# Kernel tuning notes

Hardware: AMD Instinct MI355X
Metric: run time of the kernel (lower is better)

## Reference

```python
import math
import jax, jax.numpy as jnp
import numpy as np

HIDDEN = 2048
NUM_HEADS = 32
HEAD_DIM = HIDDEN // NUM_HEADS
NUM_BLOCKS = 4
INTER = 2 * HIDDEN
EPS = 1e-5
ROPE_THETA = 10000.0


def setup_inputs() -> dict:
    key = jax.random.key(0)
    ks = jax.random.split(key, 6)
    B, S = 2, 2048
    sc = 0.02
    return {
        "x": jax.random.normal(ks[0], (B, S, HIDDEN), jnp.float32),
        "attn_norm_w": jnp.ones((HIDDEN,), jnp.float32),
        "ffn_norm_w": jnp.ones((HIDDEN,), jnp.float32),
        "w_qkv": jax.random.normal(ks[1], (3 * HIDDEN, HIDDEN), jnp.float32) * sc,
        "w_o": jax.random.normal(ks[2], (HIDDEN, HIDDEN), jnp.float32) * sc,
        "w_up": jax.random.normal(ks[3], (2 * INTER, HIDDEN), jnp.float32) * sc,
        "w_down": jax.random.normal(ks[4], (HIDDEN, INTER), jnp.float32) * sc,
    }


def _rmsnorm(x, w):
    var = jnp.mean(x * x, axis=-1, keepdims=True)
    return x * jax.lax.rsqrt(var + EPS) * w


def _rope_cache(seq_len, dim, theta, scale):
    inv_freq = 1.0 / (theta ** (jnp.arange(0, dim, 2, dtype=jnp.float32) / dim))
    t = jnp.arange(seq_len, dtype=jnp.float32) / scale
    freqs = jnp.outer(t, inv_freq)                     # [S, D/2]
    emb = jnp.concatenate([freqs, freqs], axis=-1)     # [S, D]
    return jnp.cos(emb), jnp.sin(emb)


def _apply_rope(x, cos, sin):
    # x: [B, H, S, D]
    d2 = x.shape[-1] // 2
    x1, x2 = x[..., :d2], x[..., d2:]
    rot = jnp.concatenate([-x2, x1], axis=-1)
    return x * cos[None, None] + rot * sin[None, None]


def reference(x, attn_norm_w, ffn_norm_w, w_qkv, w_o, w_up, w_down):
    B, S, _ = x.shape
    residual = x
    h = _rmsnorm(x, attn_norm_w)

    qkv = jnp.einsum('bsh,oh->bso', h, w_qkv)
    qkv = qkv.reshape(B, S, 3, NUM_HEADS, HEAD_DIM)
    q, k, v = qkv[:, :, 0], qkv[:, :, 1], qkv[:, :, 2]
    q = q.transpose(0, 2, 1, 3)  # [B,H,S,D]
    k = k.transpose(0, 2, 1, 3)
    v = v.transpose(0, 2, 1, 3)

    cos, sin = _rope_cache(S, HEAD_DIM, ROPE_THETA, 1.0)
    q = _apply_rope(q, cos, sin)
    k = _apply_rope(k, cos, sin)

    scale = 1.0 / math.sqrt(HEAD_DIM)
    attn = jnp.einsum('bhqd,bhkd->bhqk', q, k) * scale

    num_blocks = max(1, min(NUM_BLOCKS, S))
    blk = math.ceil(S / num_blocks)
    pos = jnp.arange(S)
    block_ids = pos // blk
    block_mask = block_ids[:, None] != block_ids[None, :]
    causal_mask = pos[:, None] < pos[None, :]
    invalid = causal_mask | block_mask                 # [S,S]
    mask_floor = jnp.finfo(attn.dtype).min
    attn = jnp.where(invalid[None, None], mask_floor, attn)

    attn = jax.nn.softmax(attn, axis=-1)
    context = jnp.einsum('bhqk,bhkd->bhqd', attn, v)
    context = context.transpose(0, 2, 1, 3).reshape(B, S, HIDDEN)

    x = residual + jnp.einsum('bsh,oh->bso', context, w_o)

    residual = x
    h = _rmsnorm(x, ffn_norm_w)
    up = jnp.einsum('bsh,oh->bso', h, w_up)
    gate, value = up[..., :INTER], up[..., INTER:]
    down = jnp.einsum('bsi,oi->bso', jax.nn.silu(gate) * value, w_down)
    return residual + down
```

## Files before the change

### kernel.cpp

```cpp
#include <hip/hip_runtime.h>
#include <cstdint>
#include <cstddef>

typedef __bf16 bf16x8 __attribute__((ext_vector_type(8)));
typedef __bf16 bf16x4 __attribute__((ext_vector_type(4)));
typedef float  f32x4  __attribute__((ext_vector_type(4)));

#define TOKENS  4096
#define SEQLEN  2048
#define HID     2048
#define QKV_W   6144
#define UP_W    8192
#define INTER_  4096

__device__ __forceinline__ void async16(const void* g, void* l) {
  __builtin_amdgcn_global_load_lds(
      (__attribute__((address_space(1))) void*)(g),
      (__attribute__((address_space(3))) void*)(l), 16, 0, 0);
}

__global__ __launch_bounds__(256) void cvt_kernel(const float* __restrict__ src,
                                                  __bf16* __restrict__ dst, int n4) {
  int i = blockIdx.x * 256 + threadIdx.x;
  if (i >= n4) return;
  float4 f = ((const float4*)src)[i];
  bf16x4 o;
  o[0] = (__bf16)f.x; o[1] = (__bf16)f.y; o[2] = (__bf16)f.z; o[3] = (__bf16)f.w;
  ((bf16x4*)dst)[i] = o;
}

__global__ __launch_bounds__(256) void rmsnorm_kernel(const float* __restrict__ x,
                                                      const float* __restrict__ wgt,
                                                      __bf16* __restrict__ out) {
  const int tok = blockIdx.x;
  const int t = threadIdx.x;
  const float4* xr = (const float4*)(x + (long)tok * HID);
  float4 a = xr[t], b = xr[t + 256];
  float ss = a.x*a.x + a.y*a.y + a.z*a.z + a.w*a.w
           + b.x*b.x + b.y*b.y + b.z*b.z + b.w*b.w;
  #pragma unroll
  for (int off = 32; off; off >>= 1) ss += __shfl_xor(ss, off);
  __shared__ float red[4];
  if ((t & 63) == 0) red[t >> 6] = ss;
  __syncthreads();
  float tot = red[0] + red[1] + red[2] + red[3];
  float r = rsqrtf(tot * (1.0f / HID) + 1e-5f);
  const float4* wr = (const float4*)wgt;
  float4 wa = wr[t], wb = wr[t + 256];
  bf16x4 o0, o1;
  o0[0] = (__bf16)(a.x * r * wa.x); o0[1] = (__bf16)(a.y * r * wa.y);
  o0[2] = (__bf16)(a.z * r * wa.z); o0[3] = (__bf16)(a.w * r * wa.w);
  o1[0] = (__bf16)(b.x * r * wb.x); o1[1] = (__bf16)(b.y * r * wb.y);
  o1[2] = (__bf16)(b.z * r * wb.z); o1[3] = (__bf16)(b.w * r * wb.w);
  bf16x4* orow = (bf16x4*)(out + (long)tok * HID);
  orow[t] = o0; orow[t + 256] = o1;
}

template<bool OUT_BF16, bool ADD_RES, bool ROPE, bool SILU>
__global__ __launch_bounds__(256) void gemm_bt(const __bf16* __restrict__ A, int lda,
                                               const __bf16* __restrict__ B, int ldb,
                                               void* Cv, int ldc,
                                               const float* __restrict__ Res, int K) {
  __shared__ __align__(16) __bf16 As[128 * 64];
  __shared__ __align__(16) __bf16 Bs[128 * 64];
  const int t = threadIdx.x;
  const int lane = t & 63;
  const int w = t >> 6;
  const int wm = (w >> 1) * 64, wn = (w & 1) * 64;
  const int m0 = blockIdx.y * 128;
  const int n0 = SILU ? blockIdx.x * 64 : blockIdx.x * 128;
  const int sr = t >> 3;
  const int sc = (((t & 7) ^ (sr & 7)) * 8);
  const __bf16* Ag = A + (long)(m0 + sr) * lda + sc;
  const __bf16* Bg = B + (long)(n0 + sr) * ldb + sc;
  char* lA = (char*)As + t * 16;
  char* lB = (char*)Bs + t * 16;
  const int lr = lane & 15;
  const int lq = lane >> 4;
  f32x4 acc[4][4] = {};
  for (int k0 = 0; k0 < K; k0 += 64) {
    __syncthreads();
    #pragma unroll
    for (int c = 0; c < 4; c++)
      async16(Ag + (long)(c * 32) * lda + k0, lA + c * 4096);
    #pragma unroll
    for (int c = 0; c < 4; c++) {
      const long rowoff = SILU ? (long)((c & 1) * INTER_ + (c >> 1) * 32) * ldb
                               : (long)(c * 32) * ldb;
      async16(Bg + rowoff + k0, lB + c * 4096);
    }
    __syncthreads();
    #pragma unroll
    for (int ks = 0; ks < 2; ks++) {
      const int pos = (((ks * 4 + lq) ^ (lr & 7)) * 8);
      bf16x8 af[4], bfr[4];
      #pragma unroll
      for (int i = 0; i < 4; i++)
        af[i]  = *(const bf16x8*)(As + (wm + i * 16 + lr) * 64 + pos);
      #pragma unroll
      for (int j = 0; j < 4; j++)
        bfr[j] = *(const bf16x8*)(Bs + (wn + j * 16 + lr) * 64 + pos);
      #pragma unroll
      for (int i = 0; i < 4; i++)
        #pragma unroll
        for (int j = 0; j < 4; j++)
          acc[i][j] = __builtin_amdgcn_mfma_f32_16x16x32_bf16(af[i], bfr[j], acc[i][j], 0, 0, 0);
    }
  }
  const int lq4 = lq * 4;
  if (ROPE && n0 < 4096) {
    const float invf0 = exp2f((float)(lr)      * -0.41524101186092029f);
    const float invf1 = exp2f((float)(16 + lr) * -0.41524101186092029f);
    #pragma unroll
    for (int i = 0; i < 4; i++) {
      #pragma unroll
      for (int r = 0; r < 4; r++) {
        const long row = m0 + wm + i * 16 + lq4 + r;
        const float s = (float)(int)(row & (SEQLEN - 1));
        __bf16* crow = (__bf16*)Cv + row * (long)ldc + n0 + wn + lr;
        #pragma unroll
        for (int j = 0; j < 2; j++) {
          float x1 = acc[i][j][r], x2 = acc[i][j + 2][r];
          float ang = s * (j ? invf1 : invf0);
          float sn, cs;
          __sincosf(ang, &sn, &cs);
          crow[j * 16]       = (__bf16)(x1 * cs - x2 * sn);
          crow[(j + 2) * 16] = (__bf16)(x2 * cs + x1 * sn);
        }
      }
    }
  } else if (SILU) {
    #pragma unroll
    for (int i = 0; i < 4; i++) {
      #pragma unroll
      for (int r = 0; r < 4; r++) {
        const long row = m0 + wm + i * 16 + lq4 + r;
        #pragma unroll
        for (int j = 0; j < 2; j++) {
          const long col = n0 + (wn >> 1) + j * 16 + lr;
          float g = acc[i][j][r];
          float v = acc[i][j + 2][r];
          float sg = g / (1.0f + __expf(-g));
          ((__bf16*)Cv)[row * (long)ldc + col] = (__bf16)(sg * v);
        }
      }
    }
  } else {
    #pragma unroll
    for (int i = 0; i < 4; i++) {
      #pragma unroll
      for (int r = 0; r < 4; r++) {
        const long row = m0 + wm + i * 16 + lq4 + r;
        #pragma unroll
        for (int j = 0; j < 4; j++) {
          const long col = n0 + wn + j * 16 + lr;
          float v = acc[i][j][r];
          if (ADD_RES) v += Res[row * (long)ldc + col];
          if (OUT_BF16) ((__bf16*)Cv)[row * (long)ldc + col] = (__bf16)v;
          else          ((float*)Cv)[row * (long)ldc + col] = v;
        }
      }
    }
  }
}

#define VTS 520
__global__ __launch_bounds__(256) void attn_kernel(const __bf16* __restrict__ qkv,
                                                   __bf16* __restrict__ ctx) {
  const int qt = blockIdx.x;
  const int h  = blockIdx.y;
  const int b  = blockIdx.z;
  const int w    = threadIdx.x >> 6;
  const int lane = threadIdx.x & 63;
  const int lr = lane & 15;
  const int lq = lane >> 4;
  const int q0   = qt * 64;
  const int blk0 = (q0 >> 9) << 9;
  const int nkv  = q0 + 64 - blk0;
  const long tok0 = (long)b * SEQLEN;

  const int qrow = q0 + w * 16 + lr;
  const long qoff = (tok0 + qrow) * QKV_W + h * 64 + lq * 8;
  bf16x8 qf0 = *(const bf16x8*)(qkv + qoff);
  bf16x8 qf1 = *(const bf16x8*)(qkv + qoff + 32);

  __shared__ __align__(16) __bf16 VT[64][VTS];
  __shared__ __align__(16) __bf16 Pb[4][16][48];

  {
    const int vc = (threadIdx.x & 7) * 8;
    for (int kv = threadIdx.x >> 3; kv < nkv; kv += 32) {
      bf16x8 v8 = *(const bf16x8*)(qkv + (tok0 + blk0 + kv) * QKV_W + 2 * HID + h * 64 + vc);
      #pragma unroll
      for (int i = 0; i < 8; i++) VT[vc + i][kv] = v8[i];
    }
  }
  __syncthreads();

  float m[4], l[4];
  f32x4 oacc[4] = {};
  #pragma unroll
  for (int r = 0; r < 4; r++) { m[r] = -1e30f; l[r] = 0.0f; }

  const int myrow = q0 + w * 16 + lq * 4;

  for (int kv0 = 0; kv0 < nkv; kv0 += 32) {
    f32x4 s[2];
    #pragma unroll
    for (int nt = 0; nt < 2; nt++) {
      const long koff = (tok0 + blk0 + kv0 + nt * 16 + lr) * QKV_W + HID + h * 64 + lq * 8;
      bf16x8 kf0 = *(const bf16x8*)(qkv + koff);
      bf16x8 kf1 = *(const bf16x8*)(qkv + koff + 32);
      f32x4 sa = {0.0f, 0.0f, 0.0f, 0.0f};
      sa = __builtin_amdgcn_mfma_f32_16x16x32_bf16(qf0, kf0, sa, 0, 0, 0);
      sa = __builtin_amdgcn_mfma_f32_16x16x32_bf16(qf1, kf1, sa, 0, 0, 0);
      const int kpos = blk0 + kv0 + nt * 16 + lr;
      #pragma unroll
      for (int r = 0; r < 4; r++) {
        float v = sa[r] * 0.125f;
        s[nt][r] = (kpos <= myrow + r) ? v : -1e30f;
      }
    }
    float p0[4], p1[4], alpha[4];
    #pragma unroll
    for (int r = 0; r < 4; r++) {
      float mx = fmaxf(s[0][r], s[1][r]);
      mx = fmaxf(mx, __shfl_xor(mx, 1));
      mx = fmaxf(mx, __shfl_xor(mx, 2));
      mx = fmaxf(mx, __shfl_xor(mx, 4));
      mx = fmaxf(mx, __shfl_xor(mx, 8));
      float mn = fmaxf(m[r], mx);
      alpha[r] = __expf(m[r] - mn);
      m[r] = mn;
      p0[r] = __expf(s[0][r] - mn);
      p1[r] = __expf(s[1][r] - mn);
      float rs = p0[r] + p1[r];
      rs += __shfl_xor(rs, 1);
      rs += __shfl_xor(rs, 2);
      rs += __shfl_xor(rs, 4);
      rs += __shfl_xor(rs, 8);
      l[r] = l[r] * alpha[r] + rs;
    }
    #pragma unroll
    for (int dt = 0; dt < 4; dt++)
      #pragma unroll
      for (int r = 0; r < 4; r++) oacc[dt][r] *= alpha[r];

    #pragma unroll
    for (int r = 0; r < 4; r++) {
      Pb[w][lq * 4 + r][lr]      = (__bf16)p0[r];
      Pb[w][lq * 4 + r][16 + lr] = (__bf16)p1[r];
    }
    asm volatile("s_waitcnt lgkmcnt(0)" ::: "memory");
    bf16x8 pf = *(const bf16x8*)(&Pb[w][lr][lq * 8]);
    #pragma unroll
    for (int dt = 0; dt < 4; dt++) {
      bf16x8 vf = *(const bf16x8*)(&VT[dt * 16 + lr][kv0 + lq * 8]);
      oacc[dt] = __builtin_amdgcn_mfma_f32_16x16x32_bf16(pf, vf, oacc[dt], 0, 0, 0);
    }
  }
  #pragma unroll
  for (int r = 0; r < 4; r++) {
    float inv = 1.0f / l[r];
    long obase = (tok0 + myrow + r) * HID + h * 64;
    #pragma unroll
    for (int dt = 0; dt < 4; dt++)
      ctx[obase + dt * 16 + lr] = (__bf16)(oacc[dt][r] * inv);
  }
}

extern "C" void kernel_launch(void* const* d_in, const int* in_sizes, int n_in,
                              void* d_out, int out_size, void* d_ws, size_t ws_size,
                              hipStream_t stream) {
  const float* x      = (const float*)d_in[0];
  const float* anw    = (const float*)d_in[1];
  const float* fnw    = (const float*)d_in[2];
  const float* w_qkv  = (const float*)d_in[3];
  const float* w_o    = (const float*)d_in[4];
  const float* w_up   = (const float*)d_in[5];
  const float* w_down = (const float*)d_in[6];
  float* out = (float*)d_out;

  char* wsb = (char*)d_ws;
  __bf16* ABUF = (__bf16*)wsb;
  __bf16* QKV  = (__bf16*)(wsb + (size_t)16777216);
  __bf16* WBUF = (__bf16*)(wsb + (size_t)83886080);
  __bf16* ACT  = QKV;

  rmsnorm_kernel<<<TOKENS, 256, 0, stream>>>(x, anw, ABUF);
  cvt_kernel<<<(QKV_W * HID / 4 + 255) / 256, 256, 0, stream>>>(w_qkv, WBUF, QKV_W * HID / 4);
  gemm_bt<true, false, true, false><<<dim3(QKV_W / 128, TOKENS / 128), 256, 0, stream>>>(
      ABUF, HID, WBUF, HID, (void*)QKV, QKV_W, nullptr, HID);
  attn_kernel<<<dim3(SEQLEN / 64, 32, 2), 256, 0, stream>>>(QKV, ABUF);
  cvt_kernel<<<(HID * HID / 4 + 255) / 256, 256, 0, stream>>>(w_o, WBUF, HID * HID / 4);
  gemm_bt<false, true, false, false><<<dim3(HID / 128, TOKENS / 128), 256, 0, stream>>>(
      ABUF, HID, WBUF, HID, (void*)out, HID, x, HID);

  rmsnorm_kernel<<<TOKENS, 256, 0, stream>>>(out, fnw, ABUF);
  cvt_kernel<<<(UP_W * HID / 4 + 255) / 256, 256, 0, stream>>>(w_up, WBUF, UP_W * HID / 4);
  gemm_bt<true, false, false, true><<<dim3(INTER_ / 64, TOKENS / 128), 256, 0, stream>>>(
      ABUF, HID, WBUF, HID, (void*)ACT, INTER_, nullptr, HID);
  cvt_kernel<<<(HID * INTER_ / 4 + 255) / 256, 256, 0, stream>>>(w_down, WBUF, HID * INTER_ / 4);
  gemm_bt<false, true, false, false><<<dim3(HID / 128, TOKENS / 128), 256, 0, stream>>>(
      ACT, INTER_, WBUF, INTER_, (void*)out, HID, out, INTER_);
}
```

Measured before the change: 617.9 us.

## Triple-buffer GEMM loads with 128x256 tiles, 512 threads and XCD-aware block remap

Rewrites the bf16 GEMM main loop so global-to-LDS async loads are issued two K-steps ahead into a three-stage ring buffer, waiting with vmcnt counts instead of a pair of full barriers per step. The block tile grows to 128x256 with 8 waves, and block indices are remapped in groups of 8, presumably to keep neighbouring tiles on the same XCD for L2 reuse. MFMA sections are wrapped in setprio. The aim is to hide load latency and raise operand reuse, at the cost of much more LDS (about 144KB) and register pressure, which limits occupancy.

```diff
diff --git a/kernel.cpp b/kernel.cpp
--- a/kernel.cpp
+++ b/kernel.cpp
@@ -57,56 +57,101 @@
 }
 
 template<bool OUT_BF16, bool ADD_RES, bool ROPE, bool SILU>
-__global__ __launch_bounds__(256) void gemm_bt(const __bf16* __restrict__ A, int lda,
-                                               const __bf16* __restrict__ B, int ldb,
-                                               void* Cv, int ldc,
-                                               const float* __restrict__ Res, int K) {
-  __shared__ __align__(16) __bf16 As[128 * 64];
-  __shared__ __align__(16) __bf16 Bs[128 * 64];
-  const int t = threadIdx.x;
-  const int lane = t & 63;
-  const int w = t >> 6;
-  const int wm = (w >> 1) * 64, wn = (w & 1) * 64;
-  const int m0 = blockIdx.y * 128;
-  const int n0 = SILU ? blockIdx.x * 64 : blockIdx.x * 128;
-  const int sr = t >> 3;
-  const int sc = (((t & 7) ^ (sr & 7)) * 8);
-  const __bf16* Ag = A + (long)(m0 + sr) * lda + sc;
-  const __bf16* Bg = B + (long)(n0 + sr) * ldb + sc;
-  char* lA = (char*)As + t * 16;
-  char* lB = (char*)Bs + t * 16;
-  const int lr = lane & 15;
-  const int lq = lane >> 4;
+__global__ __launch_bounds__(512, 2) void gemm_bt(const __bf16* __restrict__ A, int lda,
+                                                  const __bf16* __restrict__ B, int ldb,
+                                                  void* Cv, int ldc,
+                                                  const float* __restrict__ Res, int K) {
+  __shared__ __align__(16) __bf16 As[3 * 8192];
+  __shared__ __align__(16) __bf16 Bs[3 * 16384];
+  const int tid  = threadIdx.x;
+  const int lane = tid & 63;
+  const int w    = tid >> 6;
+  const int wm   = (w >> 2) * 64;
+  const int wn   = (w & 3) * 64;
+  const int lr   = lane & 15;
+  const int lq   = lane >> 4;
+
+  const int h   = blockIdx.y * gridDim.x + blockIdx.x;
+  const int per = (gridDim.x * gridDim.y) >> 3;
+  const int W   = (h & 7) * per + (h >> 3);
+  const int bx  = W / gridDim.y;
+  const int by  = W - bx * gridDim.y;
+  const int m0  = by * 128;
+  const int n0  = SILU ? bx * 128 : bx * 256;
+
+  const int srow = tid >> 2;
+  const int swz  = ((tid & 3) ^ ((tid >> 3) & 3)) * 8;
+  const __bf16* Ag = A + (long)(m0 + srow) * lda + swz;
+  long brow0, brow1;
+  if (SILU) {
+    const int R0 = srow, R1 = 128 + srow;
+    brow0 = (long)(((R0 >> 5) & 1) * INTER_ + n0 + (R0 >> 6) * 32 + (R0 & 31));
+    brow1 = (long)(((R1 >> 5) & 1) * INTER_ + n0 + (R1 >> 6) * 32 + (R1 & 31));
+  } else {
+    brow0 = n0 + srow;
+    brow1 = n0 + 128 + srow;
+  }
+  const __bf16* Bg0 = B + brow0 * ldb + swz;
+  const __bf16* Bg1 = B + brow1 * ldb + swz;
+  char* lA = (char*)As + tid * 16;
+  char* lB = (char*)Bs + tid * 16;
+
+#define STAGE(tt, bb) do {                                            \
+    const long ko_ = (long)(tt) * 64;                                 \
+    async16(Ag  + ko_,      lA + (bb) * 16384);                       \
+    async16(Ag  + ko_ + 32, lA + (bb) * 16384 + 8192);                \
+    async16(Bg0 + ko_,      lB + (bb) * 32768);                       \
+    async16(Bg1 + ko_,      lB + (bb) * 32768 + 8192);                \
+    async16(Bg0 + ko_ + 32, lB + (bb) * 32768 + 16384);               \
+    async16(Bg1 + ko_ + 32, lB + (bb) * 32768 + 16384 + 8192);        \
+  } while (0)
+
+  const int chx  = (lq ^ ((lr >> 1) & 3)) * 16;
+  const int aoff = (wm + lr) * 64 + chx;
+  const int boff = (wn + lr) * 64 + chx;
   f32x4 acc[4][4] = {};
-  for (int k0 = 0; k0 < K; k0 += 64) {
-    __syncthreads();
-    #pragma unroll
-    for (int c = 0; c < 4; c++)
-      async16(Ag + (long)(c * 32) * lda + k0, lA + c * 4096);
-    #pragma unroll
-    for (int c = 0; c < 4; c++) {
-      const long rowoff = SILU ? (long)((c & 1) * INTER_ + (c >> 1) * 32) * ldb
-                               : (long)(c * 32) * ldb;
-      async16(Bg + rowoff + k0, lB + c * 4096);
-    }
-    __syncthreads();
-    #pragma unroll
-    for (int ks = 0; ks < 2; ks++) {
-      const int pos = (((ks * 4 + lq) ^ (lr & 7)) * 8);
+  const int NT = K >> 6;
+
+  STAGE(0, 0);
+  STAGE(1, 1);
+  asm volatile("s_waitcnt vmcnt(6)" ::: "memory");
+  __builtin_amdgcn_sched_barrier(0);
+  __builtin_amdgcn_s_barrier();
+  asm volatile("" ::: "memory");
+
+  int bcur = 0;
+  for (int t = 0; t < NT; ++t) {
+    int bp = bcur + 2; if (bp >= 3) bp -= 3;
+    const bool pre = (t + 2 < NT);
+    if (pre) STAGE(t + 2, bp);
+    const char* Ab = (const char*)As + bcur * 16384;
+    const char* Bb = (const char*)Bs + bcur * 32768;
+    #pragma unroll
+    for (int ks = 0; ks < 2; ++ks) {
       bf16x8 af[4], bfr[4];
       #pragma unroll
       for (int i = 0; i < 4; i++)
-        af[i]  = *(const bf16x8*)(As + (wm + i * 16 + lr) * 64 + pos);
+        af[i]  = *(const bf16x8*)(Ab + ks * 8192  + aoff + i * 1024);
       #pragma unroll
       for (int j = 0; j < 4; j++)
-        bfr[j] = *(const bf16x8*)(Bs + (wn + j * 16 + lr) * 64 + pos);
+        bfr[j] = *(const bf16x8*)(Bb + ks * 16384 + boff + j * 1024);
+      __builtin_amdgcn_s_setprio(1);
       #pragma unroll
       for (int i = 0; i < 4; i++)
         #pragma unroll
         for (int j = 0; j < 4; j++)
           acc[i][j] = __builtin_amdgcn_mfma_f32_16x16x32_bf16(af[i], bfr[j], acc[i][j], 0, 0, 0);
-    }
-  }
+      __builtin_amdgcn_s_setprio(0);
+    }
+    if (pre) asm volatile("s_waitcnt vmcnt(6)" ::: "memory");
+    else     asm volatile("s_waitcnt vmcnt(0)" ::: "memory");
+    __builtin_amdgcn_sched_barrier(0);
+    __builtin_amdgcn_s_barrier();
+    asm volatile("" ::: "memory");
+    bcur = (bcur == 2) ? 0 : bcur + 1;
+  }
+#undef STAGE
+
   const int lq4 = lq * 4;
   if (ROPE && n0 < 4096) {
     const float invf0 = exp2f((float)(lr)      * -0.41524101186092029f);
@@ -289,18 +334,18 @@
 
   rmsnorm_kernel<<<TOKENS, 256, 0, stream>>>(x, anw, ABUF);
   cvt_kernel<<<(QKV_W * HID / 4 + 255) / 256, 256, 0, stream>>>(w_qkv, WBUF, QKV_W * HID / 4);
-  gemm_bt<true, false, true, false><<<dim3(QKV_W / 128, TOKENS / 128), 256, 0, stream>>>(
+  gemm_bt<true, false, true, false><<<dim3(QKV_W / 256, TOKENS / 128), 512, 0, stream>>>(
       ABUF, HID, WBUF, HID, (void*)QKV, QKV_W, nullptr, HID);
   attn_kernel<<<dim3(SEQLEN / 64, 32, 2), 256, 0, stream>>>(QKV, ABUF);
   cvt_kernel<<<(HID * HID / 4 + 255) / 256, 256, 0, stream>>>(w_o, WBUF, HID * HID / 4);
-  gemm_bt<false, true, false, false><<<dim3(HID / 128, TOKENS / 128), 256, 0, stream>>>(
+  gemm_bt<false, true, false, false><<<dim3(HID / 256, TOKENS / 128), 512, 0, stream>>>(
       ABUF, HID, WBUF, HID, (void*)out, HID, x, HID);
 
   rmsnorm_kernel<<<TOKENS, 256, 0, stream>>>(out, fnw, ABUF);
   cvt_kernel<<<(UP_W * HID / 4 + 255) / 256, 256, 0, stream>>>(w_up, WBUF, UP_W * HID / 4);
-  gemm_bt<true, false, false, true><<<dim3(INTER_ / 64, TOKENS / 128), 256, 0, stream>>>(
+  gemm_bt<true, false, false, true><<<dim3(INTER_ / 128, TOKENS / 128), 512, 0, stream>>>(
       ABUF, HID, WBUF, HID, (void*)ACT, INTER_, nullptr, HID);
   cvt_kernel<<<(HID * INTER_ / 4 + 255) / 256, 256, 0, stream>>>(w_down, WBUF, HID * INTER_ / 4);
-  gemm_bt<false, true, false, false><<<dim3(HID / 128, TOKENS / 128), 256, 0, stream>>>(
+  gemm_bt<false, true, false, false><<<dim3(HID / 256, TOKENS / 128), 512, 0, stream>>>(
       ACT, INTER_, WBUF, INTER_, (void*)out, HID, out, INTER_);
 }
```

Result: slower. 743.8 us (+20.4%).

## Add 256x256 eight-wave pipelined GEMM for QKV and gate-up projections

Applied to the files above, without the earlier changes.

Adds a new GEMM kernel with 512 threads and a 256x256 output tile (256x128 for the fused SiLU path). It double-buffers LDS with async global-to-LDS loads interleaved between quarter-tile MFMA phases, uses explicit waitcnt and barrier scheduling, and raises MFMA priority with s_setprio. The QKV (with RoPE) and gate/up (with SiLU) GEMMs switch to it, aiming for more data reuse per tile and better overlap of memory with compute. In exchange it uses 128KB of LDS per block and many more accumulator registers, which can lower occupancy.

```diff
diff --git a/kernel.cpp b/kernel.cpp
--- a/kernel.cpp
+++ b/kernel.cpp
@@ -108,56 +108,196 @@
     }
   }
   const int lq4 = lq * 4;
-  if (ROPE && n0 < 4096) {
-    const float invf0 = exp2f((float)(lr)      * -0.41524101186092029f);
-    const float invf1 = exp2f((float)(16 + lr) * -0.41524101186092029f);
-    #pragma unroll
-    for (int i = 0; i < 4; i++) {
-      #pragma unroll
-      for (int r = 0; r < 4; r++) {
-        const long row = m0 + wm + i * 16 + lq4 + r;
-        const float s = (float)(int)(row & (SEQLEN - 1));
-        __bf16* crow = (__bf16*)Cv + row * (long)ldc + n0 + wn + lr;
+  #pragma unroll
+  for (int i = 0; i < 4; i++) {
+    #pragma unroll
+    for (int r = 0; r < 4; r++) {
+      const long row = m0 + wm + i * 16 + lq4 + r;
+      #pragma unroll
+      for (int j = 0; j < 4; j++) {
+        const long col = n0 + wn + j * 16 + lr;
+        float v = acc[i][j][r];
+        if (ADD_RES) v += Res[row * (long)ldc + col];
+        if (OUT_BF16) ((__bf16*)Cv)[row * (long)ldc + col] = (__bf16)v;
+        else          ((float*)Cv)[row * (long)ldc + col] = v;
+      }
+    }
+  }
+}
+
+template<bool ROPE, bool SILU>
+__global__ __launch_bounds__(512, 2) void gemm8p(const __bf16* __restrict__ A, int lda,
+                                                 const __bf16* __restrict__ B, int ldb,
+                                                 void* Cv, int ldc, int K) {
+  __shared__ __align__(16) __bf16 As[2 * 16384];
+  __shared__ __align__(16) __bf16 Bs[2 * 16384];
+  const int tid  = threadIdx.x;
+  const int lane = tid & 63;
+  const int w    = tid >> 6;
+  const int wm2  = w >> 2;
+  const int wn4  = w & 3;
+  const int lr   = lane & 15;
+  const int lq   = lane >> 4;
+  const int m0   = blockIdx.y * 256;
+  const int n0   = ROPE ? blockIdx.x * 256 : 0;
+  const int n0c  = SILU ? blockIdx.x * 128 : 0;
+
+  const long r0 = tid >> 3;
+  const int  e  = (((tid & 7) ^ ((int)r0 & 7)) * 8);
+  const __bf16* Ap0 = A + (long)(m0 + r0) * lda + e;
+  long br0, br1, bhs;
+  if (ROPE) {
+    br0 = n0 + 64 * (((int)r0 >> 5) & 3) + ((int)r0 & 31);
+    br1 = n0 + 64 * ((((int)r0 + 64) >> 5) & 3) + ((int)r0 & 31);
+    bhs = 32 * (long)ldb;
+  } else {
+    br0 = n0c + r0;
+    br1 = n0c + r0 + 64;
+    bhs = (long)INTER_ * ldb;
+  }
+  const __bf16* Bp0 = B + br0 * ldb + e;
+  const __bf16* Bp1 = B + br1 * ldb + e;
+  char* sA = (char*)As;
+  char* sB = (char*)Bs;
+  const int tid16 = tid * 16;
+
+#define STAGE_A(h_, nb_, kk_) do {                                                     \
+    async16(Ap0 + (long)((h_) * 128) * lda + (kk_),      sA + (nb_)*32768 + (h_)*16384 + tid16);        \
+    async16(Ap0 + (long)((h_) * 128 + 64) * lda + (kk_), sA + (nb_)*32768 + (h_)*16384 + 8192 + tid16); \
+  } while (0)
+#define STAGE_B(h_, nb_, kk_) do {                                                     \
+    async16(Bp0 + (h_) * bhs + (kk_), sB + (nb_)*32768 + (h_)*16384 + tid16);          \
+    async16(Bp1 + (h_) * bhs + (kk_), sB + (nb_)*32768 + (h_)*16384 + 8192 + tid16);   \
+  } while (0)
+
+  const int ch0 = ((lq ^ (lr & 7)) * 16);
+  const int ch1 = (((4 + lq) ^ (lr & 7)) * 16);
+  const int abase = (wm2 * 64 + lr) * 128;
+  const int bbase = (wn4 * 32 + lr) * 128;
+
+  f32x4 acc[8][4] = {};
+  bf16x8 af[4][2], bfr[4][2];
+  const int NT = K >> 6;
+
+#define LOAD_A(mh_) do {                                                               \
+    _Pragma("unroll")                                                                  \
+    for (int i = 0; i < 4; i++) {                                                      \
+      af[i][0] = *(const bf16x8*)(Ab + abase + (mh_)*16384 + i*2048 + ch0);            \
+      af[i][1] = *(const bf16x8*)(Ab + abase + (mh_)*16384 + i*2048 + ch1);            \
+    } } while (0)
+#define LOAD_B(nh_) do {                                                               \
+    _Pragma("unroll")                                                                  \
+    for (int j = 0; j < 2; j++) {                                                      \
+      bfr[(nh_)*2 + j][0] = *(const bf16x8*)(Bb + bbase + (nh_)*16384 + j*2048 + ch0); \
+      bfr[(nh_)*2 + j][1] = *(const bf16x8*)(Bb + bbase + (nh_)*16384 + j*2048 + ch1); \
+    } } while (0)
+#define MFMA_Q(mh_, nh_) do {                                                          \
+    __builtin_amdgcn_s_setprio(1);                                                     \
+    _Pragma("unroll")                                                                  \
+    for (int ks = 0; ks < 2; ks++)                                                     \
+      _Pragma("unroll")                                                                \
+      for (int i = 0; i < 4; i++)                                                      \
+        _Pragma("unroll")                                                              \
+        for (int j = 0; j < 2; j++)                                                    \
+          acc[(mh_)*4 + i][(nh_)*2 + j] = __builtin_amdgcn_mfma_f32_16x16x32_bf16(     \
+              af[i][ks], bfr[(nh_)*2 + j][ks], acc[(mh_)*4 + i][(nh_)*2 + j], 0, 0, 0);\
+    __builtin_amdgcn_s_setprio(0);                                                     \
+  } while (0)
+#define SBAR() do { __builtin_amdgcn_sched_barrier(0);                                 \
+    __builtin_amdgcn_s_barrier(); __builtin_amdgcn_sched_barrier(0); } while (0)
+#define LGKM0() do { asm volatile("s_waitcnt lgkmcnt(0)" ::: "memory");                \
+    __builtin_amdgcn_sched_barrier(0); } while (0)
+
+  STAGE_A(0, 0, 0); STAGE_B(0, 0, 0); STAGE_B(1, 0, 0); STAGE_A(1, 0, 0);
+  asm volatile("s_waitcnt vmcnt(4)" ::: "memory");
+  SBAR();
+
+  for (int T = 0; T < NT; ++T) {
+    const int cb = T & 1, nb = cb ^ 1;
+    const int kk = (T + 1) << 6;
+    const bool st = (T + 1 < NT);
+    const char* Ab = (const char*)As + cb * 32768;
+    const char* Bb = (const char*)Bs + cb * 32768;
+    LOAD_A(0); LOAD_B(0);
+    if (st) { STAGE_A(0, nb, kk); STAGE_B(0, nb, kk); }
+    SBAR(); LGKM0();
+    MFMA_Q(0, 0);
+    if (st) asm volatile("s_waitcnt vmcnt(6)" ::: "memory");
+    else    asm volatile("s_waitcnt vmcnt(2)" ::: "memory");
+    SBAR();
+    LOAD_B(1);
+    if (st) STAGE_B(1, nb, kk);
+    SBAR(); LGKM0();
+    MFMA_Q(0, 1);
+    if (st) asm volatile("s_waitcnt vmcnt(6)" ::: "memory");
+    else    asm volatile("s_waitcnt vmcnt(0)" ::: "memory");
+    SBAR();
+    LOAD_A(1);
+    if (st) STAGE_A(1, nb, kk);
+    SBAR(); LGKM0();
+    MFMA_Q(1, 0);
+    SBAR();
+    MFMA_Q(1, 1);
+    if (st) asm volatile("s_waitcnt vmcnt(4)" ::: "memory");
+    SBAR();
+  }
+#undef STAGE_A
+#undef STAGE_B
+#undef LOAD_A
+#undef LOAD_B
+#undef MFMA_Q
+#undef SBAR
+#undef LGKM0
+
+  const int lq4 = lq * 4;
+  if (ROPE) {
+    if (n0 < 4096) {
+      const float invf0 = exp2f((float)(lr)      * -0.41524101186092029f);
+      const float invf1 = exp2f((float)(16 + lr) * -0.41524101186092029f);
+      #pragma unroll
+      for (int mi = 0; mi < 8; mi++) {
         #pragma unroll
-        for (int j = 0; j < 2; j++) {
-          float x1 = acc[i][j][r], x2 = acc[i][j + 2][r];
-          float ang = s * (j ? invf1 : invf0);
-          float sn, cs;
-          __sincosf(ang, &sn, &cs);
-          crow[j * 16]       = (__bf16)(x1 * cs - x2 * sn);
-          crow[(j + 2) * 16] = (__bf16)(x2 * cs + x1 * sn);
+        for (int r = 0; r < 4; r++) {
+          const long row = m0 + (mi >> 2) * 128 + wm2 * 64 + (mi & 3) * 16 + lq4 + r;
+          const float s = (float)(int)(row & (SEQLEN - 1));
+          __bf16* crow = (__bf16*)Cv + row * (long)ldc + n0 + wn4 * 64 + lr;
+          #pragma unroll
+          for (int nj = 0; nj < 2; nj++) {
+            float x1 = acc[mi][nj][r], x2 = acc[mi][nj + 2][r];
+            float ang = s * (nj ? invf1 : invf0);
+            float sn, cs;
+            __sincosf(ang, &sn, &cs);
+            crow[nj * 16]      = (__bf16)(x1 * cs - x2 * sn);
+            crow[nj * 16 + 32] = (__bf16)(x2 * cs + x1 * sn);
+          }
         }
       }
-    }
-  } else if (SILU) {
-    #pragma unroll
-    for (int i = 0; i < 4; i++) {
+    } else {
+      #pragma unroll
+      for (int mi = 0; mi < 8; mi++) {
+        #pragma unroll
+        for (int r = 0; r < 4; r++) {
+          const long row = m0 + (mi >> 2) * 128 + wm2 * 64 + (mi & 3) * 16 + lq4 + r;
+          __bf16* crow = (__bf16*)Cv + row * (long)ldc + n0 + wn4 * 64 + lr;
+          #pragma unroll
+          for (int njf = 0; njf < 4; njf++)
+            crow[(njf >> 1) * 32 + (njf & 1) * 16] = (__bf16)acc[mi][njf][r];
+        }
+      }
+    }
+  } else {
+    #pragma unroll
+    for (int mi = 0; mi < 8; mi++) {
       #pragma unroll
       for (int r = 0; r < 4; r++) {
-        const long row = m0 + wm + i * 16 + lq4 + r;
+        const long row = m0 + (mi >> 2) * 128 + wm2 * 64 + (mi & 3) * 16 + lq4 + r;
         #pragma unroll
-        for (int j = 0; j < 2; j++) {
-          const long col = n0 + (wn >> 1) + j * 16 + lr;
-          float g = acc[i][j][r];
-          float v = acc[i][j + 2][r];
+        for (int nj = 0; nj < 2; nj++) {
+          const long col = n0c + wn4 * 32 + nj * 16 + lr;
+          float g = acc[mi][nj][r];
+          float v = acc[mi][nj + 2][r];
           float sg = g / (1.0f + __expf(-g));
           ((__bf16*)Cv)[row * (long)ldc + col] = (__bf16)(sg * v);
-        }
-      }
-    }
-  } else {
-    #pragma unroll
-    for (int i = 0; i < 4; i++) {
-      #pragma unroll
-      for (int r = 0; r < 4; r++) {
-        const long row = m0 + wm + i * 16 + lq4 + r;
-        #pragma unroll
-        for (int j = 0; j < 4; j++) {
-          const long col = n0 + wn + j * 16 + lr;
-          float v = acc[i][j][r];
-          if (ADD_RES) v += Res[row * (long)ldc + col];
-          if (OUT_BF16) ((__bf16*)Cv)[row * (long)ldc + col] = (__bf16)v;
-          else          ((float*)Cv)[row * (long)ldc + col] = v;
         }
       }
     }
@@ -289,8 +429,8 @@
 
   rmsnorm_kernel<<<TOKENS, 256, 0, stream>>>(x, anw, ABUF);
   cvt_kernel<<<(QKV_W * HID / 4 + 255) / 256, 256, 0, stream>>>(w_qkv, WBUF, QKV_W * HID / 4);
-  gemm_bt<true, false, true, false><<<dim3(QKV_W / 128, TOKENS / 128), 256, 0, stream>>>(
-      ABUF, HID, WBUF, HID, (void*)QKV, QKV_W, nullptr, HID);
+  gemm8p<true, false><<<dim3(QKV_W / 256, TOKENS / 256), 512, 0, stream>>>(
+      ABUF, HID, WBUF, HID, (void*)QKV, QKV_W, HID);
   attn_kernel<<<dim3(SEQLEN / 64, 32, 2), 256, 0, stream>>>(QKV, ABUF);
   cvt_kernel<<<(HID * HID / 4 + 255) / 256, 256, 0, stream>>>(w_o, WBUF, HID * HID / 4);
   gemm_bt<false, true, false, false><<<dim3(HID / 128, TOKENS / 128), 256, 0, stream>>>(
@@ -298,8 +438,8 @@
 
   rmsnorm_kernel<<<TOKENS, 256, 0, stream>>>(out, fnw, ABUF);
   cvt_kernel<<<(UP_W * HID / 4 + 255) / 256, 256, 0, stream>>>(w_up, WBUF, UP_W * HID / 4);
-  gemm_bt<true, false, false, true><<<dim3(INTER_ / 64, TOKENS / 128), 256, 0, stream>>>(
-      ABUF, HID, WBUF, HID, (void*)ACT, INTER_, nullptr, HID);
+  gemm8p<false, true><<<dim3(INTER_ / 128, TOKENS / 256), 512, 0, stream>>>(
+      ABUF, HID, WBUF, HID, (void*)ACT, INTER_, HID);
   cvt_kernel<<<(HID * INTER_ / 4 + 255) / 256, 256, 0, stream>>>(w_down, WBUF, HID * INTER_ / 4);
   gemm_bt<false, true, false, false><<<dim3(HID / 128, TOKENS / 128), 256, 0, stream>>>(
       ACT, INTER_, WBUF, INTER_, (void*)out, HID, out, INTER_);
```

Result: faster. 589.3 us (-4.6%).
